# Kernel optimization log

Hardware: AMD Instinct MI355X
Metric: run time of the kernel (lower is better)

## Reference

```python
import jax, jax.numpy as jnp
import numpy as np

B, C, H, W = 2, 256, 64, 64  # C = in_channels; x has 2*C channels
DQ = C // 16


def setup_inputs() -> dict:
    key = jax.random.key(0)
    ks = jax.random.split(key, 10)
    s = 0.05
    return {
        "x": jax.random.normal(ks[0], (B, 2 * C, H, W), dtype=jnp.float32),
        "Wq": jax.random.normal(ks[1], (DQ, C), dtype=jnp.float32) * s,
        "bq": jax.random.normal(ks[2], (DQ,), dtype=jnp.float32) * s,
        "Wk": jax.random.normal(ks[3], (DQ, C), dtype=jnp.float32) * s,
        "bk": jax.random.normal(ks[4], (DQ,), dtype=jnp.float32) * s,
        "Wv": jax.random.normal(ks[5], (C, C), dtype=jnp.float32) * s,
        "bv": jax.random.normal(ks[6], (C,), dtype=jnp.float32) * s,
        "Wpt": jax.random.normal(ks[7], (C, 2 * C), dtype=jnp.float32) * s,
        "bpt": jax.random.normal(ks[8], (C,), dtype=jnp.float32) * s,
        "gamma": jnp.full((1,), 0.5, dtype=jnp.float32),  # original inits to 0; nonzero for a non-trivial output
    }


def _conv1x1(x, Wt, b):
    # 1x1 conv == per-pixel linear map over channels
    return jnp.einsum("bchw,dc->bdhw", x, Wt) + b[None, :, None, None]


def reference(x, Wq, bq, Wk, bk, Wv, bv, Wpt, bpt, gamma):
    n = x.shape[1] // 2
    x1, x2 = x[:, :n], x[:, n:]
    b, c, h, w = x1.shape
    hw = h * w

    def qkv(xi):
        q = _conv1x1(xi, Wq, bq).reshape(b, DQ, hw)   # [B,dq,HW]
        k = _conv1x1(xi, Wk, bk).reshape(b, DQ, hw)   # [B,dq,HW]
        v = _conv1x1(xi, Wv, bv).reshape(b, c, hw)    # [B,C,HW]
        return q, k, v

    q1, k1, v1 = qkv(x1)
    q2, k2, v2 = qkv(x2)

    # attn[b,i,j] = softmax_j( q[:,i] . k[:,j] )  (no scaling, as in original)
    attn1 = jax.nn.softmax(jnp.einsum("bdi,bdj->bij", q1, k1), axis=-1)  # [B,HW,HW]
    attn2 = jax.nn.softmax(jnp.einsum("bdi,bdj->bij", q2, k2), axis=-1)

    def apply_attn(v, attn):
        # out[b,c,i] = sum_j v[b,c,j] * attn[b,i,j]
        return jnp.einsum("bcj,bij->bci", v, attn).reshape(b, c, h, w)

    out11 = apply_attn(v1, attn1)
    out12 = apply_attn(v2, attn1)
    out21 = apply_attn(v1, attn2)
    out22 = apply_attn(v2, attn2)

    o1 = _conv1x1(jnp.concatenate([out11, out12], axis=1), Wpt, bpt)  # [B,C,H,W]
    o2 = _conv1x1(jnp.concatenate([out21, out22], axis=1), Wpt, bpt)

    out = gamma * jnp.concatenate([o1, o2], axis=1) + x
    return out
```

## Files before the change

### kernel.cpp

```cpp
#include <hip/hip_runtime.h>
#include <hip/hip_bf16.h>


#define HW 4096
#define CC 256
#define DQ 16

typedef __hip_bfloat16 bf16;
struct alignas(8) bh4 { bf16 x, y, z, w; };
typedef __bf16 bf16x8 __attribute__((ext_vector_type(8)));
typedef float  f32x4  __attribute__((ext_vector_type(4)));

static __device__ __forceinline__ float b2f(bf16 v) { return __bfloat162float(v); }

static __device__ __forceinline__ void load_lds16(const void* g, void* l) {
    __builtin_amdgcn_global_load_lds(
        (const __attribute__((address_space(1))) unsigned int*)g,
        (__attribute__((address_space(3))) unsigned int*)l, 16, 0, 0);
}

static __device__ __forceinline__ bf16x8 ones8() {
    union { unsigned int u[4]; bf16x8 v; } t;
    t.u[0] = t.u[1] = t.u[2] = t.u[3] = 0x3F803F80u;
    return t.v;
}

struct ConvArgs { const void* src[9]; float* dst[9]; int n[9]; };
__global__ void convert_weights(ConvArgs a, const unsigned short* __restrict__ probe) {
    int seg = blockIdx.y;
    int i = blockIdx.x * 256 + threadIdx.x;
    bool isb = probe[0] != 0;
    if (i < a.n[seg])
        a.dst[seg][i] = isb ? b2f(((const bf16*)a.src[seg])[i])
                            : ((const float*)a.src[seg])[i];
}

__global__ void w_to_bf16(const float* __restrict__ Wqf, const float* __restrict__ Wkf,
                          bf16* __restrict__ Wqb, bf16* __restrict__ Wkb) {
    int i = blockIdx.x * 256 + threadIdx.x;
    const float* s = blockIdx.y ? Wkf : Wqf;
    bf16* d = blockIdx.y ? Wkb : Wqb;
    d[i] = __float2bfloat16(s[i]);
}

__global__ void convert_x_t(const void* __restrict__ xsrc, bf16* __restrict__ Xt,
                            const unsigned short* __restrict__ probe) {
    __shared__ float T[64][65];
    int t = threadIdx.x;
    int j0 = blockIdx.x * 64, e0 = blockIdx.y * 64, b = blockIdx.z;
    bool isb = probe[0] != 0;
    int j_l = t & 63, er0 = (t >> 6) * 16;
#pragma unroll
    for (int r = 0; r < 16; ++r) {
        size_t src = ((size_t)(b * 512 + e0 + er0 + r)) * HW + j0 + j_l;
        T[er0 + r][j_l] = isb ? b2f(((const bf16*)xsrc)[src]) : ((const float*)xsrc)[src];
    }
    __syncthreads();
    int e_w = t & 63, jr0 = (t >> 6) * 16;
#pragma unroll
    for (int r = 0; r < 16; ++r)
        Xt[((size_t)b * HW + j0 + jr0 + r) * 512 + e0 + e_w] = __float2bfloat16(T[e_w][jr0 + r]);
}

__global__ void build_mc(const float* __restrict__ Wv, const float* __restrict__ bv,
                         const float* __restrict__ Wpt, const float* __restrict__ bpt,
                         bf16* __restrict__ McB, float* __restrict__ btot) {
    int blk = blockIdx.x, tid = threadIdx.x;
    if (blk < 512) {
        int d = blk >> 1;
        int c = ((blk & 1) << 8) + tid;
        int half = c >> 8, cm = c & 255;
        float acc = 0.f;
        for (int e = 0; e < 256; ++e)
            acc = fmaf(Wpt[d * 512 + half * 256 + e], Wv[e * 256 + cm], acc);
        McB[d * 512 + c] = __float2bfloat16(acc);
    } else {
        int d = tid;
        float acc = bpt[d];
        for (int e = 0; e < 256; ++e)
            acc = fmaf(Wpt[d * 512 + e] + Wpt[d * 512 + 256 + e], bv[e], acc);
        btot[d] = acc;
    }
}

__global__ void __launch_bounds__(256)
build_qk_mfma(const bf16* __restrict__ Xt,
              const bf16* __restrict__ Wqb, const float* __restrict__ bqf,
              const bf16* __restrict__ Wkb, const float* __restrict__ bkf,
              bf16* __restrict__ Qb, bf16* __restrict__ Kb) {
    int tid = threadIdx.x;
    int lane = tid & 63, wave = tid >> 6;
    int ln = lane & 15, q = lane >> 4;
    int bh = blockIdx.y;
    int b = bh >> 1, h = bh & 1;
    int j0 = blockIdx.x * 64 + wave * 16;

    bf16x8 aQ[8], aK[8];
#pragma unroll
    for (int kk = 0; kk < 8; ++kk) {
        aQ[kk] = *(const bf16x8*)&Wqb[ln * 256 + kk * 32 + q * 8];
        aK[kk] = *(const bf16x8*)&Wkb[ln * 256 + kk * 32 + q * 8];
    }
    const bf16* Xrow = Xt + ((size_t)b * HW + j0 + ln) * 512 + h * 256;
    f32x4 dQ = {0.f, 0.f, 0.f, 0.f}, dK = {0.f, 0.f, 0.f, 0.f};
#pragma unroll
    for (int kk = 0; kk < 8; ++kk) {
        bf16x8 bx = *(const bf16x8*)&Xrow[kk * 32 + q * 8];
        dQ = __builtin_amdgcn_mfma_f32_16x16x32_bf16(aQ[kk], bx, dQ, 0, 0, 0);
        dK = __builtin_amdgcn_mfma_f32_16x16x32_bf16(aK[kk], bx, dK, 0, 0, 0);
    }
    size_t rowoff = ((size_t)bh * HW + j0 + ln) * 32;
    bh4 oq, ok;
    oq.x = __float2bfloat16(dQ[0] + bqf[q * 4 + 0]);
    oq.y = __float2bfloat16(dQ[1] + bqf[q * 4 + 1]);
    oq.z = __float2bfloat16(dQ[2] + bqf[q * 4 + 2]);
    oq.w = __float2bfloat16(dQ[3] + bqf[q * 4 + 3]);
    ok.x = __float2bfloat16(dK[0] + bkf[q * 4 + 0]);
    ok.y = __float2bfloat16(dK[1] + bkf[q * 4 + 1]);
    ok.z = __float2bfloat16(dK[2] + bkf[q * 4 + 2]);
    ok.w = __float2bfloat16(dK[3] + bkf[q * 4 + 3]);
    bh4 z; z.x = z.y = z.z = z.w = __float2bfloat16(0.f);
    *(bh4*)&Qb[rowoff + q * 4] = oq;
    *(bh4*)&Qb[rowoff + 16 + q * 4] = z;
    *(bh4*)&Kb[rowoff + q * 4] = ok;
    *(bh4*)&Kb[rowoff + 16 + q * 4] = z;
}

__global__ void __launch_bounds__(256, 2)
build_u_mfma(const bf16* __restrict__ McB, const bf16* __restrict__ Xt,
             bf16* __restrict__ Ub) {
    __shared__ __align__(16) bf16 sA[64 * 64];
    __shared__ __align__(16) bf16 sB[128 * 64];
    int tid = threadIdx.x;
    int lane = tid & 63, wave = tid >> 6;
    int ln = lane & 15, q = lane >> 4;
    int wm = (wave >> 1) * 32, wn = (wave & 1) * 64;
    int j0 = blockIdx.x * 128, c0 = blockIdx.y * 64, b = blockIdx.z;
    const bf16* Xb = Xt + (size_t)b * HW * 512;
    f32x4 acc[2][4];
#pragma unroll
    for (int mi = 0; mi < 2; ++mi)
#pragma unroll
        for (int ni = 0; ni < 4; ++ni)
#pragma unroll
            for (int r = 0; r < 4; ++r) acc[mi][ni][r] = 0.f;

    for (int e0 = 0; e0 < 512; e0 += 64) {
        __syncthreads();
#pragma unroll
        for (int r = 0; r < 2; ++r) {
            int s = r * 256 + tid;
            int row = s >> 3, jc = s & 7, jg = jc ^ (row & 7);
            load_lds16(McB + (size_t)(c0 + row) * 512 + e0 + jg * 8, sA + s * 8);
        }
#pragma unroll
        for (int r = 0; r < 4; ++r) {
            int s = r * 256 + tid;
            int row = s >> 3, jc = s & 7, jg = jc ^ (row & 7);
            load_lds16(Xb + (size_t)(j0 + row) * 512 + e0 + jg * 8, sB + s * 8);
        }
        __syncthreads();
#pragma unroll
        for (int kh = 0; kh < 2; ++kh) {
            bf16x8 af[2], bfv[4];
#pragma unroll
            for (int mi = 0; mi < 2; ++mi) {
                int row = wm + mi * 16 + ln;
                int jc = (kh * 4 + q) ^ (row & 7);
                af[mi] = *(const bf16x8*)&sA[row * 64 + jc * 8];
            }
#pragma unroll
            for (int ni = 0; ni < 4; ++ni) {
                int row = wn + ni * 16 + ln;
                int jc = (kh * 4 + q) ^ (row & 7);
                bfv[ni] = *(const bf16x8*)&sB[row * 64 + jc * 8];
            }
#pragma unroll
            for (int mi = 0; mi < 2; ++mi)
#pragma unroll
                for (int ni = 0; ni < 4; ++ni)
                    acc[mi][ni] = __builtin_amdgcn_mfma_f32_16x16x32_bf16(
                        af[mi], bfv[ni], acc[mi][ni], 0, 0, 0);
        }
    }
#pragma unroll
    for (int mi = 0; mi < 2; ++mi)
#pragma unroll
        for (int r = 0; r < 4; ++r) {
            int c = c0 + wm + mi * 16 + q * 4 + r;
#pragma unroll
            for (int ni = 0; ni < 4; ++ni) {
                int j = j0 + wn + ni * 16 + ln;
                Ub[((size_t)(b * CC + c)) * HW + j] = __float2bfloat16(acc[mi][ni][r]);
            }
        }
}

__global__ void __launch_bounds__(256, 2)
flash_attn(const bf16* __restrict__ Ub, const bf16* __restrict__ Qb,
           const bf16* __restrict__ Kb, const float* __restrict__ btot,
           const void* __restrict__ xorig, const float* __restrict__ gamf,
           void* __restrict__ outv, const unsigned short* __restrict__ probe) {
    __shared__ __align__(16) bf16 sU[2][128 * 64];
    __shared__ __align__(16) bf16 sE[2][64 * 64];
    int tid  = threadIdx.x;
    int lane = tid & 63, wave = tid >> 6;
    int ln = lane & 15, q = lane >> 4;
    int wm = (wave & 1) * 64, wn = (wave >> 1) * 32;
    int i0 = blockIdx.x * 64, c0 = blockIdx.y * 128;
    int bh = blockIdx.z;
    int b = bh >> 1, h = bh & 1;
    const bf16* Ubb = Ub + (size_t)b * CC * HW + (size_t)c0 * HW;
    const bf16* Kbh = Kb + (size_t)bh * HW * 32;
    const bf16x8 ONE = ones8();

    bf16x8 bq = *(const bf16x8*)&Qb[((size_t)bh * HW + i0 + wave * 16 + ln) * 32 + q * 8];

    f32x4 acc[4][2], accS[2];
#pragma unroll
    for (int ni = 0; ni < 2; ++ni) {
#pragma unroll
        for (int r = 0; r < 4; ++r) accS[ni][r] = 0.f;
#pragma unroll
        for (int mi = 0; mi < 4; ++mi)
#pragma unroll
            for (int r = 0; r < 4; ++r) acc[mi][ni][r] = 0.f;
    }

    int i_loc = wave * 16 + ln;
    int wchunk0 = (q >> 1);
    int woff = (q & 1) * 4;

    auto stageU = [&](int buf, int j0) {
#pragma unroll
        for (int r = 0; r < 4; ++r) {
            int s = r * 256 + tid;
            int row = s >> 3, jc = s & 7, jg = jc ^ (row & 7);
            load_lds16(Ubb + (size_t)row * HW + j0 + jg * 8, &sU[buf][s * 8]);
        }
    };
    auto qkTile = [&](int buf, int j0) {
#pragma unroll
        for (int js = 0; js < 4; ++js) {
            bf16x8 ak = *(const bf16x8*)&Kbh[(size_t)(j0 + js * 16 + ln) * 32 + q * 8];
            f32x4 d = {0.f, 0.f, 0.f, 0.f};
            d = __builtin_amdgcn_mfma_f32_16x16x32_bf16(ak, bq, d, 0, 0, 0);
            bh4 o;
            o.x = __float2bfloat16(__expf(d[0]));
            o.y = __float2bfloat16(__expf(d[1]));
            o.z = __float2bfloat16(__expf(d[2]));
            o.w = __float2bfloat16(__expf(d[3]));
            int chunk = (js * 2 + wchunk0) ^ (i_loc & 7);
            *(bh4*)&sE[buf][i_loc * 64 + chunk * 8 + woff] = o;
        }
    };

    stageU(0, 0);
    qkTile(0, 0);

    for (int t = 0; t < 64; ++t) {
        int cur = t & 1, nxt = cur ^ 1;
        __syncthreads();
        if (t < 63) {
            stageU(nxt, (t + 1) * 64);
            qkTile(nxt, (t + 1) * 64);
        }
#pragma unroll
        for (int kh = 0; kh < 2; ++kh) {
            bf16x8 af[4], bfv[2];
#pragma unroll
            for (int mi = 0; mi < 4; ++mi) {
                int row = wm + mi * 16 + ln;
                int jc = (kh * 4 + q) ^ (row & 7);
                af[mi] = *(const bf16x8*)&sU[cur][row * 64 + jc * 8];
            }
#pragma unroll
            for (int ni = 0; ni < 2; ++ni) {
                int row = wn + ni * 16 + ln;
                int jc = (kh * 4 + q) ^ (row & 7);
                bfv[ni] = *(const bf16x8*)&sE[cur][row * 64 + jc * 8];
            }
#pragma unroll
            for (int ni = 0; ni < 2; ++ni) {
                accS[ni] = __builtin_amdgcn_mfma_f32_16x16x32_bf16(
                    ONE, bfv[ni], accS[ni], 0, 0, 0);
#pragma unroll
                for (int mi = 0; mi < 4; ++mi)
                    acc[mi][ni] = __builtin_amdgcn_mfma_f32_16x16x32_bf16(
                        af[mi], bfv[ni], acc[mi][ni], 0, 0, 0);
            }
        }
    }

    bool isb = probe[0] != 0;
    float g = gamf[0];
    float lv[2];
#pragma unroll
    for (int ni = 0; ni < 2; ++ni)
        lv[ni] = 1.f / accS[ni][0];
#pragma unroll
    for (int mi = 0; mi < 4; ++mi)
#pragma unroll
        for (int r = 0; r < 4; ++r) {
            int c = c0 + wm + mi * 16 + q * 4 + r;
            float bt = btot[c];
            size_t rowbase = ((size_t)(b * 512 + h * 256 + c)) * HW + i0 + wn;
#pragma unroll
            for (int ni = 0; ni < 2; ++ni) {
                size_t idx = rowbase + ni * 16 + ln;
                float xres = isb ? b2f(((const bf16*)xorig)[idx]) : ((const float*)xorig)[idx];
                float o = fmaf(g, fmaf(acc[mi][ni][r], lv[ni], bt), xres);
                if (isb) ((bf16*)outv)[idx] = __float2bfloat16(o);
                else     ((float*)outv)[idx] = o;
            }
        }
}

extern "C" void kernel_launch(void* const* d_in, const int* in_sizes, int n_in,
                              void* d_out, int out_size, void* d_ws, size_t ws_size,
                              hipStream_t stream) {
    const unsigned short* probe = (const unsigned short*)d_in[9];

    char* ws = (char*)d_ws;
    size_t off = 0;
    auto alloc = [&](size_t bytes) { size_t r = off; off = (off + bytes + 255) & ~(size_t)255; return r; };
    const int wsz[9] = {DQ * 256, DQ, DQ * 256, DQ, 256 * 256, 256, 256 * 512, 256, 1};
    float* wf[9];
    for (int t = 0; t < 9; ++t) wf[t] = (float*)(ws + alloc((size_t)wsz[t] * 4));
    bf16*  Xt   = (bf16*)(ws + alloc((size_t)2 * HW * 512 * 2));
    bf16*  McB  = (bf16*)(ws + alloc(256 * 512 * 2));
    float* btot = (float*)(ws + alloc(256 * 4));
    bf16*  Wqb  = (bf16*)(ws + alloc(DQ * 256 * 2));
    bf16*  Wkb  = (bf16*)(ws + alloc(DQ * 256 * 2));
    bf16*  Qb   = (bf16*)(ws + alloc((size_t)4 * HW * 32 * 2));
    bf16*  Kb   = (bf16*)(ws + alloc((size_t)4 * HW * 32 * 2));
    bf16*  Ub   = (bf16*)(ws + alloc((size_t)2 * CC * HW * 2));

    ConvArgs ca;
    for (int t = 0; t < 9; ++t) { ca.src[t] = d_in[t + 1]; ca.dst[t] = wf[t]; ca.n[t] = wsz[t]; }
    convert_weights<<<dim3(512, 9), 256, 0, stream>>>(ca, probe);
    w_to_bf16<<<dim3(16, 2), 256, 0, stream>>>(wf[0], wf[2], Wqb, Wkb);
    convert_x_t<<<dim3(64, 8, 2), 256, 0, stream>>>(d_in[0], Xt, probe);

    build_mc<<<513, 256, 0, stream>>>(wf[4], wf[5], wf[6], wf[7], McB, btot);
    build_qk_mfma<<<dim3(64, 4), 256, 0, stream>>>(Xt, Wqb, wf[1], Wkb, wf[3], Qb, Kb);
    build_u_mfma<<<dim3(32, 4, 2), 256, 0, stream>>>(McB, Xt, Ub);

    flash_attn<<<dim3(64, 2, 4), 256, 0, stream>>>(Ub, Qb, Kb, btot, d_in[0], wf[8], d_out, probe);
}
```

Measured before the change: 208.7 us.

## Fuse weight prep kernels and give each wave private exp tiles in flash attention

The separate weight conversion, bf16 cast and Mc/btot build kernels are merged into one prep kernel that reads raw inputs directly, cutting launches and the intermediate fp32 weight copies. In flash_attn, each wave now computes and consumes its own 16-row exp(QK) tile in a private LDS slice, so the exp tile no longer needs double buffering or a block barrier before use. Each wave covers all 128 channels for its 16 query rows, which means 8 U fragments are read from LDS per k-step instead of 4 U plus 2 E. The QK MFMA and exp work now sits on the critical path rather than being prefetched one tile ahead, and the accumulator and register layout changes.

```diff
diff --git a/kernel.cpp b/kernel.cpp
--- a/kernel.cpp
+++ b/kernel.cpp
@@ -25,22 +25,52 @@
     return t.v;
 }
 
-struct ConvArgs { const void* src[9]; float* dst[9]; int n[9]; };
-__global__ void convert_weights(ConvArgs a, const unsigned short* __restrict__ probe) {
-    int seg = blockIdx.y;
-    int i = blockIdx.x * 256 + threadIdx.x;
+__global__ void prep_all(const void* __restrict__ Wq_r, const void* __restrict__ bq_r,
+                         const void* __restrict__ Wk_r, const void* __restrict__ bk_r,
+                         const void* __restrict__ Wv_r, const void* __restrict__ bv_r,
+                         const void* __restrict__ Wpt_r, const void* __restrict__ bpt_r,
+                         const void* __restrict__ gam_r,
+                         const unsigned short* __restrict__ probe,
+                         bf16* __restrict__ McB, float* __restrict__ btot,
+                         bf16* __restrict__ Wqb, bf16* __restrict__ Wkb,
+                         float* __restrict__ bqf, float* __restrict__ bkf,
+                         float* __restrict__ gamf) {
     bool isb = probe[0] != 0;
-    if (i < a.n[seg])
-        a.dst[seg][i] = isb ? b2f(((const bf16*)a.src[seg])[i])
-                            : ((const float*)a.src[seg])[i];
-}
-
-__global__ void w_to_bf16(const float* __restrict__ Wqf, const float* __restrict__ Wkf,
-                          bf16* __restrict__ Wqb, bf16* __restrict__ Wkb) {
-    int i = blockIdx.x * 256 + threadIdx.x;
-    const float* s = blockIdx.y ? Wkf : Wqf;
-    bf16* d = blockIdx.y ? Wkb : Wqb;
-    d[i] = __float2bfloat16(s[i]);
+    int blk = blockIdx.x, tid = threadIdx.x;
+    auto ldf = [&](const void* p, int i) -> float {
+        return isb ? b2f(((const bf16*)p)[i]) : ((const float*)p)[i];
+    };
+    if (blk < 512) {
+        int d = blk >> 1;
+        int c = ((blk & 1) << 8) + tid;
+        int half = c >> 8, cm = c & 255;
+        float acc = 0.f;
+        if (isb) {
+            const bf16* wp = (const bf16*)Wpt_r;
+            const bf16* wv = (const bf16*)Wv_r;
+            for (int e = 0; e < 256; ++e)
+                acc = fmaf(b2f(wp[d * 512 + half * 256 + e]), b2f(wv[e * 256 + cm]), acc);
+        } else {
+            const float* wp = (const float*)Wpt_r;
+            const float* wv = (const float*)Wv_r;
+            for (int e = 0; e < 256; ++e)
+                acc = fmaf(wp[d * 512 + half * 256 + e], wv[e * 256 + cm], acc);
+        }
+        McB[d * 512 + c] = __float2bfloat16(acc);
+    } else if (blk == 512) {
+        int d = tid;
+        float acc = ldf(bpt_r, d);
+        for (int e = 0; e < 256; ++e)
+            acc = fmaf(ldf(Wpt_r, d * 512 + e) + ldf(Wpt_r, d * 512 + 256 + e), ldf(bv_r, e), acc);
+        btot[d] = acc;
+    } else {
+        for (int k = tid; k < DQ * 256; k += 256) {
+            Wqb[k] = isb ? ((const bf16*)Wq_r)[k] : __float2bfloat16(((const float*)Wq_r)[k]);
+            Wkb[k] = isb ? ((const bf16*)Wk_r)[k] : __float2bfloat16(((const float*)Wk_r)[k]);
+        }
+        if (tid < DQ) { bqf[tid] = ldf(bq_r, tid); bkf[tid] = ldf(bk_r, tid); }
+        if (tid == DQ) gamf[0] = ldf(gam_r, 0);
+    }
 }
 
 __global__ void convert_x_t(const void* __restrict__ xsrc, bf16* __restrict__ Xt,
@@ -60,27 +90,6 @@
 #pragma unroll
     for (int r = 0; r < 16; ++r)
         Xt[((size_t)b * HW + j0 + jr0 + r) * 512 + e0 + e_w] = __float2bfloat16(T[e_w][jr0 + r]);
-}
-
-__global__ void build_mc(const float* __restrict__ Wv, const float* __restrict__ bv,
-                         const float* __restrict__ Wpt, const float* __restrict__ bpt,
-                         bf16* __restrict__ McB, float* __restrict__ btot) {
-    int blk = blockIdx.x, tid = threadIdx.x;
-    if (blk < 512) {
-        int d = blk >> 1;
-        int c = ((blk & 1) << 8) + tid;
-        int half = c >> 8, cm = c & 255;
-        float acc = 0.f;
-        for (int e = 0; e < 256; ++e)
-            acc = fmaf(Wpt[d * 512 + half * 256 + e], Wv[e * 256 + cm], acc);
-        McB[d * 512 + c] = __float2bfloat16(acc);
-    } else {
-        int d = tid;
-        float acc = bpt[d];
-        for (int e = 0; e < 256; ++e)
-            acc = fmaf(Wpt[d * 512 + e] + Wpt[d * 512 + 256 + e], bv[e], acc);
-        btot[d] = acc;
-    }
 }
 
 __global__ void __launch_bounds__(256)
@@ -202,33 +211,29 @@
            const void* __restrict__ xorig, const float* __restrict__ gamf,
            void* __restrict__ outv, const unsigned short* __restrict__ probe) {
     __shared__ __align__(16) bf16 sU[2][128 * 64];
-    __shared__ __align__(16) bf16 sE[2][64 * 64];
+    __shared__ __align__(16) bf16 sE[4][16 * 64];
     int tid  = threadIdx.x;
     int lane = tid & 63, wave = tid >> 6;
     int ln = lane & 15, q = lane >> 4;
-    int wm = (wave & 1) * 64, wn = (wave >> 1) * 32;
     int i0 = blockIdx.x * 64, c0 = blockIdx.y * 128;
     int bh = blockIdx.z;
     int b = bh >> 1, h = bh & 1;
     const bf16* Ubb = Ub + (size_t)b * CC * HW + (size_t)c0 * HW;
     const bf16* Kbh = Kb + (size_t)bh * HW * 32;
     const bf16x8 ONE = ones8();
+    bf16* sEw = &sE[wave][0];
 
     bf16x8 bq = *(const bf16x8*)&Qb[((size_t)bh * HW + i0 + wave * 16 + ln) * 32 + q * 8];
 
-    f32x4 acc[4][2], accS[2];
-#pragma unroll
-    for (int ni = 0; ni < 2; ++ni) {
-#pragma unroll
-        for (int r = 0; r < 4; ++r) accS[ni][r] = 0.f;
-#pragma unroll
-        for (int mi = 0; mi < 4; ++mi)
-#pragma unroll
-            for (int r = 0; r < 4; ++r) acc[mi][ni][r] = 0.f;
-    }
-
-    int i_loc = wave * 16 + ln;
-    int wchunk0 = (q >> 1);
+    f32x4 acc[8], accS;
+#pragma unroll
+    for (int r = 0; r < 4; ++r) accS[r] = 0.f;
+#pragma unroll
+    for (int mi = 0; mi < 8; ++mi)
+#pragma unroll
+        for (int r = 0; r < 4; ++r) acc[mi][r] = 0.f;
+
+    int wchunk0 = q >> 1;
     int woff = (q & 1) * 4;
 
     auto stageU = [&](int buf, int j0) {
@@ -239,7 +244,14 @@
             load_lds16(Ubb + (size_t)row * HW + j0 + jg * 8, &sU[buf][s * 8]);
         }
     };
-    auto qkTile = [&](int buf, int j0) {
+
+    stageU(0, 0);
+
+    for (int t = 0; t < 64; ++t) {
+        int cur = t & 1;
+        __syncthreads();
+        if (t < 63) stageU(cur ^ 1, (t + 1) * 64);
+        int j0 = t * 64;
 #pragma unroll
         for (int js = 0; js < 4; ++js) {
             bf16x8 ak = *(const bf16x8*)&Kbh[(size_t)(j0 + js * 16 + ln) * 32 + q * 8];
@@ -250,69 +262,38 @@
             o.y = __float2bfloat16(__expf(d[1]));
             o.z = __float2bfloat16(__expf(d[2]));
             o.w = __float2bfloat16(__expf(d[3]));
-            int chunk = (js * 2 + wchunk0) ^ (i_loc & 7);
-            *(bh4*)&sE[buf][i_loc * 64 + chunk * 8 + woff] = o;
-        }
-    };
-
-    stageU(0, 0);
-    qkTile(0, 0);
-
-    for (int t = 0; t < 64; ++t) {
-        int cur = t & 1, nxt = cur ^ 1;
-        __syncthreads();
-        if (t < 63) {
-            stageU(nxt, (t + 1) * 64);
-            qkTile(nxt, (t + 1) * 64);
+            int chunk = (js * 2 + wchunk0) ^ (ln & 7);
+            *(bh4*)&sEw[ln * 64 + chunk * 8 + woff] = o;
         }
 #pragma unroll
         for (int kh = 0; kh < 2; ++kh) {
-            bf16x8 af[4], bfv[2];
-#pragma unroll
-            for (int mi = 0; mi < 4; ++mi) {
-                int row = wm + mi * 16 + ln;
+            int jcE = (kh * 4 + q) ^ (ln & 7);
+            bf16x8 bfv = *(const bf16x8*)&sEw[ln * 64 + jcE * 8];
+            accS = __builtin_amdgcn_mfma_f32_16x16x32_bf16(ONE, bfv, accS, 0, 0, 0);
+#pragma unroll
+            for (int mi = 0; mi < 8; ++mi) {
+                int row = mi * 16 + ln;
                 int jc = (kh * 4 + q) ^ (row & 7);
-                af[mi] = *(const bf16x8*)&sU[cur][row * 64 + jc * 8];
-            }
-#pragma unroll
-            for (int ni = 0; ni < 2; ++ni) {
-                int row = wn + ni * 16 + ln;
-                int jc = (kh * 4 + q) ^ (row & 7);
-                bfv[ni] = *(const bf16x8*)&sE[cur][row * 64 + jc * 8];
-            }
-#pragma unroll
-            for (int ni = 0; ni < 2; ++ni) {
-                accS[ni] = __builtin_amdgcn_mfma_f32_16x16x32_bf16(
-                    ONE, bfv[ni], accS[ni], 0, 0, 0);
-#pragma unroll
-                for (int mi = 0; mi < 4; ++mi)
-                    acc[mi][ni] = __builtin_amdgcn_mfma_f32_16x16x32_bf16(
-                        af[mi], bfv[ni], acc[mi][ni], 0, 0, 0);
+                bf16x8 af = *(const bf16x8*)&sU[cur][row * 64 + jc * 8];
+                acc[mi] = __builtin_amdgcn_mfma_f32_16x16x32_bf16(af, bfv, acc[mi], 0, 0, 0);
             }
         }
     }
 
     bool isb = probe[0] != 0;
     float g = gamf[0];
-    float lv[2];
-#pragma unroll
-    for (int ni = 0; ni < 2; ++ni)
-        lv[ni] = 1.f / accS[ni][0];
-#pragma unroll
-    for (int mi = 0; mi < 4; ++mi)
+    float lv = 1.f / accS[0];
+    int i = i0 + wave * 16 + ln;
+#pragma unroll
+    for (int mi = 0; mi < 8; ++mi)
 #pragma unroll
         for (int r = 0; r < 4; ++r) {
-            int c = c0 + wm + mi * 16 + q * 4 + r;
-            float bt = btot[c];
-            size_t rowbase = ((size_t)(b * 512 + h * 256 + c)) * HW + i0 + wn;
-#pragma unroll
-            for (int ni = 0; ni < 2; ++ni) {
-                size_t idx = rowbase + ni * 16 + ln;
-                float xres = isb ? b2f(((const bf16*)xorig)[idx]) : ((const float*)xorig)[idx];
-                float o = fmaf(g, fmaf(acc[mi][ni][r], lv[ni], bt), xres);
-                if (isb) ((bf16*)outv)[idx] = __float2bfloat16(o);
-                else     ((float*)outv)[idx] = o;
-            }
+            int c = c0 + mi * 16 + q * 4 + r;
+            size_t idx = ((size_t)(b * 512 + h * 256 + c)) * HW + i;
+            float xres = isb ? b2f(((const bf16*)xorig)[idx]) : ((const float*)xorig)[idx];
+            float o = fmaf(g, fmaf(acc[mi][r], lv, btot[c]), xres);
+            if (isb) ((bf16*)outv)[idx] = __float2bfloat16(o);
+            else     ((float*)outv)[idx] = o;
         }
 }
 
@@ -324,27 +305,25 @@
     char* ws = (char*)d_ws;
     size_t off = 0;
     auto alloc = [&](size_t bytes) { size_t r = off; off = (off + bytes + 255) & ~(size_t)255; return r; };
-    const int wsz[9] = {DQ * 256, DQ, DQ * 256, DQ, 256 * 256, 256, 256 * 512, 256, 1};
-    float* wf[9];
-    for (int t = 0; t < 9; ++t) wf[t] = (float*)(ws + alloc((size_t)wsz[t] * 4));
     bf16*  Xt   = (bf16*)(ws + alloc((size_t)2 * HW * 512 * 2));
     bf16*  McB  = (bf16*)(ws + alloc(256 * 512 * 2));
     float* btot = (float*)(ws + alloc(256 * 4));
     bf16*  Wqb  = (bf16*)(ws + alloc(DQ * 256 * 2));
     bf16*  Wkb  = (bf16*)(ws + alloc(DQ * 256 * 2));
+    float* bqf  = (float*)(ws + alloc(DQ * 4));
+    float* bkf  = (float*)(ws + alloc(DQ * 4));
+    float* gamf = (float*)(ws + alloc(4));
     bf16*  Qb   = (bf16*)(ws + alloc((size_t)4 * HW * 32 * 2));
     bf16*  Kb   = (bf16*)(ws + alloc((size_t)4 * HW * 32 * 2));
     bf16*  Ub   = (bf16*)(ws + alloc((size_t)2 * CC * HW * 2));
 
-    ConvArgs ca;
-    for (int t = 0; t < 9; ++t) { ca.src[t] = d_in[t + 1]; ca.dst[t] = wf[t]; ca.n[t] = wsz[t]; }
-    convert_weights<<<dim3(512, 9), 256, 0, stream>>>(ca, probe);
-    w_to_bf16<<<dim3(16, 2), 256, 0, stream>>>(wf[0], wf[2], Wqb, Wkb);
+    prep_all<<<514, 256, 0, stream>>>(d_in[1], d_in[2], d_in[3], d_in[4], d_in[5],
+                                      d_in[6], d_in[7], d_in[8], d_in[9], probe,
+                                      McB, btot, Wqb, Wkb, bqf, bkf, gamf);
     convert_x_t<<<dim3(64, 8, 2), 256, 0, stream>>>(d_in[0], Xt, probe);
 
-    build_mc<<<513, 256, 0, stream>>>(wf[4], wf[5], wf[6], wf[7], McB, btot);
-    build_qk_mfma<<<dim3(64, 4), 256, 0, stream>>>(Xt, Wqb, wf[1], Wkb, wf[3], Qb, Kb);
+    build_qk_mfma<<<dim3(64, 4), 256, 0, stream>>>(Xt, Wqb, bqf, Wkb, bkf, Qb, Kb);
     build_u_mfma<<<dim3(32, 4, 2), 256, 0, stream>>>(McB, Xt, Ub);
 
-    flash_attn<<<dim3(64, 2, 4), 256, 0, stream>>>(Ub, Qb, Kb, btot, d_in[0], wf[8], d_out, probe);
-}
+    flash_attn<<<dim3(64, 2, 4), 256, 0, stream>>>(Ub, Qb, Kb, btot, d_in[0], gamf, d_out, probe);
+}
```

Result: slower. 249.9 us (+19.7%).
